# Kernel optimization log

Hardware: AMD Instinct MI355X
Metric: run time of the kernel (lower is better)

## Reference

```python
import jax, jax.numpy as jnp
import numpy as np

NUM_USERS = 1024
NUM_BUSINESSES = 2048
N_NODES = NUM_USERS + NUM_BUSINESSES  # 3072
B = 1024            # batch size (== NUM_USERS to keep the business_idx-offset bug valid)
E = 16384           # edges (self loops added inside reference, PyG GATConv default)
H = 768             # hidden_size
HEADS = 8
NUM_IMAGES = 3


def setup_inputs() -> dict:
    key = jax.random.key(0)
    ks = jax.random.split(key, 24)
    def rn(k, shape, s=0.02):
        return jax.random.normal(k, shape, dtype=jnp.float32) * s
    inp = {
        'text_cls': rn(ks[0], (B, 768), 1.0),              # BERT CLS features
        'img_cls': rn(ks[1], (B, NUM_IMAGES, 768), 1.0),   # ViT CLS features per image
        'biz_feats': rn(ks[2], (B, 3), 1.0),
        'W_text': rn(ks[3], (768, H)), 'b_text': jnp.zeros((H,), jnp.float32),
        'W_img': rn(ks[4], (768, H)), 'b_img': jnp.zeros((H,), jnp.float32),
        'W_bf': rn(ks[5], (3, H)), 'b_bf': jnp.zeros((H,), jnp.float32),
        'user_table': rn(ks[6], (NUM_USERS, H)),
        'biz_table': rn(ks[7], (NUM_BUSINESSES, H)),
        'W1': rn(ks[8], (H, HEADS * H)),
        'att_src1': rn(ks[9], (HEADS, H), 0.1),
        'att_dst1': rn(ks[10], (HEADS, H), 0.1),
        'b1': jnp.zeros((HEADS * H,), jnp.float32),
        'W2': rn(ks[11], (HEADS * H, H)),
        'att_src2': rn(ks[12], (1, H), 0.1),
        'att_dst2': rn(ks[13], (1, H), 0.1),
        'b2': jnp.zeros((H,), jnp.float32),
        'Wf1': rn(ks[14], (4 * H, 2 * H)), 'bf1': jnp.zeros((2 * H,), jnp.float32),
        'Wf2': rn(ks[15], (2 * H, H)), 'bf2': jnp.zeros((H,), jnp.float32),
        'Wf3': rn(ks[16], (H, 1)), 'bf3': jnp.zeros((1,), jnp.float32),
        'user_idx': jax.random.randint(ks[17], (B,), 0, NUM_USERS),
        'business_idx': jax.random.randint(ks[18], (B,), NUM_USERS, N_NODES),
        'edge_index': jax.random.randint(ks[19], (2, E), 0, N_NODES),
    }
    return inp


def gat_conv(x, src, dst, W, a_src, a_dst, bias, heads):
    # PyG GATConv: linear -> per-head additive attention -> scatter softmax over dst -> scatter add
    N = x.shape[0]
    C = W.shape[1] // heads
    h = (x @ W).reshape(N, heads, C)                       # [N,H,C]
    s_src = jnp.sum(h * a_src, axis=-1)                    # [N,H]
    s_dst = jnp.sum(h * a_dst, axis=-1)                    # [N,H]
    e = jax.nn.leaky_relu(s_src[src] + s_dst[dst], 0.2)    # [E,H]
    e_max = jax.ops.segment_max(e, dst, num_segments=N)    # [N,H]
    ee = jnp.exp(e - e_max[dst])
    denom = jax.ops.segment_sum(ee, dst, num_segments=N)   # [N,H]
    alpha = ee / (denom[dst] + 1e-16)                      # [E,H]
    out = jax.ops.segment_sum(h[src] * alpha[..., None], dst, num_segments=N)  # [N,H,C]
    return out.reshape(N, heads * C) + bias


def reference(text_cls, img_cls, biz_feats, W_text, b_text, W_img, b_img, W_bf, b_bf,
              user_table, biz_table, W1, att_src1, att_dst1, b1, W2, att_src2, att_dst2, b2,
              Wf1, bf1, Wf2, bf2, Wf3, bf3, user_idx, business_idx, edge_index):
    text_emb = text_cls @ W_text + b_text                       # TextEncoder.fc
    img_emb = jnp.mean(img_cls, axis=1) @ W_img + b_img         # ImageEncoder mean + fc
    meta = biz_feats @ W_bf + b_bf                              # business_feature_fc
    user_emb = user_table[user_idx]
    biz_emb = biz_table[business_idx - user_idx.shape[0]]       # faithful: offset by batch size
    x = jnp.zeros((N_NODES, H), jnp.float32)
    x = x.at[user_idx].set(user_emb)
    x = x.at[business_idx].set((text_emb + img_emb + meta + biz_emb) / 4.0)
    loop = jnp.arange(N_NODES)
    src = jnp.concatenate([edge_index[0], loop])                # add self loops (PyG default)
    dst = jnp.concatenate([edge_index[1], loop])
    x = jax.nn.relu(gat_conv(x, src, dst, W1, att_src1, att_dst1, b1, HEADS))
    x = gat_conv(x, src, dst, W2, att_src2, att_dst2, b2, 1)
    cat = jnp.concatenate([x[user_idx], x[business_idx], text_emb, img_emb], axis=1)  # [B,4H]
    h1 = jax.nn.relu(cat @ Wf1 + bf1)
    h2 = jax.nn.relu(h1 @ Wf2 + bf2)
    return (h2 @ Wf3 + bf3).squeeze(-1)                         # [B]
```

## Files before the change

kernel.cpp:

```cpp
#include <hip/hip_runtime.h>
#include <hip/hip_bf16.h>

namespace {

constexpr int kB = 1024;
constexpr int kNU = 1024;
constexpr int kNB = 2048;
constexpr int kNN = 3072;
constexpr int kE = 16384;
constexpr int kET = kE + kNN;
constexpr int kH = 768;
constexpr int kHeads = 8;
constexpr int kS2 = 8;

typedef __attribute__((ext_vector_type(8))) short bf16x8_t;
typedef __attribute__((ext_vector_type(4))) float f32x4_t;

__device__ __forceinline__ float tof(float x) { return x; }
__device__ __forceinline__ float tof(__hip_bfloat16 x) { return __bfloat162float(x); }
__device__ __forceinline__ void stor(float* p, float v) { *p = v; }
__device__ __forceinline__ void stor(__hip_bfloat16* p, float v) { *p = __float2bfloat16(v); }

__device__ __forceinline__ float blo(unsigned u) {
  union { unsigned u; float f; } c; c.u = u << 16; return c.f;
}
__device__ __forceinline__ float bhi(unsigned u) {
  union { unsigned u; float f; } c; c.u = u & 0xffff0000u; return c.f;
}

__device__ __forceinline__ unsigned pk2(float a, float b) {
  union { __hip_bfloat16 h[2]; unsigned u; } c;
  c.h[0] = __float2bfloat16(a); c.h[1] = __float2bfloat16(b);
  return c.u;
}

__device__ __forceinline__ void gload_lds16(const void* g, void* l) {
  __builtin_amdgcn_global_load_lds(
      (const __attribute__((address_space(1))) void*)g,
      (__attribute__((address_space(3))) void*)l, 16, 0, 0);
}

template <int BM, int BN, int FM, int FN, typename TC>
__device__ __forceinline__ void gemm_body(
    const __hip_bfloat16* __restrict__ A, const __hip_bfloat16* __restrict__ Bt,
    const float* __restrict__ bias, TC* __restrict__ C,
    int K, int lda, int ldc, int act, int bx, int by) {
  __shared__ __align__(16) __hip_bfloat16 As[2][BM][32];
  __shared__ __align__(16) __hip_bfloat16 Bs[2][BN][32];
  const int t = threadIdx.x;
  const int w = t >> 6, lane = t & 63;
  const int wm = w >> 1, wn = w & 1;
  const int bm = by * BM, bn = bx * BN;
  const int lr = lane & 15, lg = lane >> 4;

  f32x4_t acc[FM][FN];
#pragma unroll
  for (int m = 0; m < FM; ++m)
#pragma unroll
    for (int n = 0; n < FN; ++n) acc[m][n] = (f32x4_t){0.f, 0.f, 0.f, 0.f};

  auto stage = [&](int buf, int kt) {
    const int k0 = kt << 5;
#pragma unroll
    for (int i = 0; i < BM / 64; ++i) {
      int L = i * 256 + t;
      gload_lds16(A + (size_t)(bm + (L >> 2)) * lda + k0 + (L & 3) * 8,
                  (char*)(&As[buf][0][0]) + ((size_t)(i * 256 + w * 64)) * 16);
    }
#pragma unroll
    for (int i = 0; i < BN / 64; ++i) {
      int L = i * 256 + t;
      gload_lds16(Bt + (size_t)(bn + (L >> 2)) * K + k0 + (L & 3) * 8,
                  (char*)(&Bs[buf][0][0]) + ((size_t)(i * 256 + w * 64)) * 16);
    }
  };

  const int NT = K >> 5;
  stage(0, 0);
  __syncthreads();
  for (int kt = 0; kt < NT; ++kt) {
    const int cur = kt & 1;
    if (kt + 1 < NT) stage(cur ^ 1, kt + 1);
    bf16x8_t af[FM], bv[FN];
#pragma unroll
    for (int m = 0; m < FM; ++m)
      af[m] = *(const bf16x8_t*)&As[cur][wm * FM * 16 + m * 16 + lr][lg * 8];
#pragma unroll
    for (int n = 0; n < FN; ++n)
      bv[n] = *(const bf16x8_t*)&Bs[cur][wn * FN * 16 + n * 16 + lr][lg * 8];
#pragma unroll
    for (int m = 0; m < FM; ++m)
#pragma unroll
      for (int n = 0; n < FN; ++n)
        acc[m][n] = __builtin_amdgcn_mfma_f32_16x16x32_bf16(af[m], bv[n], acc[m][n], 0, 0, 0);
    __syncthreads();
  }

#pragma unroll
  for (int m = 0; m < FM; ++m) {
    const int row0 = bm + wm * FM * 16 + m * 16 + lg * 4;
#pragma unroll
    for (int n = 0; n < FN; ++n) {
      const int cn = bn + wn * FN * 16 + n * 16 + lr;
      const float bvv = bias ? bias[cn] : 0.f;
#pragma unroll
      for (int r = 0; r < 4; ++r) {
        float v = acc[m][n][r] + bvv;
        if (act) v = fmaxf(v, 0.f);
        stor(&C[(size_t)(row0 + r) * ldc + cn], v);
      }
    }
  }
}

__device__ __forceinline__ void swz_xy(bool mfast, int& bx, int& by) {
  const int nwg = gridDim.x * gridDim.y;
  const int orig = blockIdx.y * gridDim.x + blockIdx.x;
  const int swz = (orig & 7) * (nwg >> 3) + (orig >> 3);
  if (mfast) { by = swz % gridDim.y; bx = swz / gridDim.y; }
  else       { bx = swz % gridDim.x; by = swz / gridDim.x; }
}

template <int BM, int BN, int FM, int FN>
__global__ __launch_bounds__(256) void mfma_gemm_dual(
    const __hip_bfloat16* __restrict__ A0, const __hip_bfloat16* __restrict__ Bt0,
    const float* __restrict__ bias0, float* __restrict__ C0,
    const __hip_bfloat16* __restrict__ A1, const __hip_bfloat16* __restrict__ Bt1,
    const float* __restrict__ bias1, float* __restrict__ C1,
    int N, int K) {
  int bx, by;
  swz_xy(true, bx, by);
  const __hip_bfloat16* A = blockIdx.z ? A1 : A0;
  const __hip_bfloat16* Bt = blockIdx.z ? Bt1 : Bt0;
  const float* bias = blockIdx.z ? bias1 : bias0;
  float* C = blockIdx.z ? C1 : C0;
  gemm_body<BM, BN, FM, FN, float>(A, Bt, bias, C, K, K, N, 0, bx, by);
}

template <int BM, int BN, int FM, int FN>
__global__ __launch_bounds__(256) void gemm_head(
    const __hip_bfloat16* __restrict__ y, const __hip_bfloat16* __restrict__ W1t,
    const float* __restrict__ b1, __hip_bfloat16* __restrict__ x2) {
  const int hd = blockIdx.x;
  const int tile = blockIdx.y;
  const int bx = tile % (kH / BN);
  const int by = tile / (kH / BN);
  gemm_body<BM, BN, FM, FN, __hip_bfloat16>(
      y + (size_t)hd * kH, W1t + (size_t)hd * kH * kH, b1 + hd * kH,
      x2 + (size_t)hd * kH, kH, kHeads * kH, kHeads * kH, 1, bx, by);
}

template <int BM, int BN, int FM, int FN, int S>
__global__ __launch_bounds__(256) void mfma_gemm_kpin(
    const __hip_bfloat16* __restrict__ A, const __hip_bfloat16* __restrict__ Bt,
    __hip_bfloat16* __restrict__ Cpart, int M, int N, int K) {
  __shared__ __align__(16) __hip_bfloat16 As[2][BM][32];
  __shared__ __align__(16) __hip_bfloat16 Bs[2][BN][32];
  const int kc = blockIdx.x;
  const int tile = blockIdx.y;
  const int tilesN = N / BN;
  const int bx = tile % tilesN;
  const int by = tile / tilesN;
  const int KC = K / S;
  const int kbeg = kc * KC;
  const int t = threadIdx.x;
  const int w = t >> 6, lane = t & 63;
  const int wm = w >> 1, wn = w & 1;
  const int bm = by * BM, bn = bx * BN;
  const int lr = lane & 15, lg = lane >> 4;

  f32x4_t acc[FM][FN];
#pragma unroll
  for (int m = 0; m < FM; ++m)
#pragma unroll
    for (int n = 0; n < FN; ++n) acc[m][n] = (f32x4_t){0.f, 0.f, 0.f, 0.f};

  auto stage = [&](int buf, int kt) {
    const int k0 = kbeg + (kt << 5);
#pragma unroll
    for (int i = 0; i < BM / 64; ++i) {
      int L = i * 256 + t;
      gload_lds16(A + (size_t)(bm + (L >> 2)) * K + k0 + (L & 3) * 8,
                  (char*)(&As[buf][0][0]) + ((size_t)(i * 256 + w * 64)) * 16);
    }
#pragma unroll
    for (int i = 0; i < BN / 64; ++i) {
      int L = i * 256 + t;
      gload_lds16(Bt + (size_t)(bn + (L >> 2)) * K + k0 + (L & 3) * 8,
                  (char*)(&Bs[buf][0][0]) + ((size_t)(i * 256 + w * 64)) * 16);
    }
  };

  const int NT = KC >> 5;
  stage(0, 0);
  __syncthreads();
  for (int kt = 0; kt < NT; ++kt) {
    const int cur = kt & 1;
    if (kt + 1 < NT) stage(cur ^ 1, kt + 1);
    bf16x8_t af[FM], bv[FN];
#pragma unroll
    for (int m = 0; m < FM; ++m)
      af[m] = *(const bf16x8_t*)&As[cur][wm * FM * 16 + m * 16 + lr][lg * 8];
#pragma unroll
    for (int n = 0; n < FN; ++n)
      bv[n] = *(const bf16x8_t*)&Bs[cur][wn * FN * 16 + n * 16 + lr][lg * 8];
#pragma unroll
    for (int m = 0; m < FM; ++m)
#pragma unroll
      for (int n = 0; n < FN; ++n)
        acc[m][n] = __builtin_amdgcn_mfma_f32_16x16x32_bf16(af[m], bv[n], acc[m][n], 0, 0, 0);
    __syncthreads();
  }

  __hip_bfloat16* Cp = Cpart + (size_t)kc * M * N;
#pragma unroll
  for (int m = 0; m < FM; ++m) {
    const int row0 = bm + wm * FM * 16 + m * 16 + lg * 4;
#pragma unroll
    for (int n = 0; n < FN; ++n) {
      const int cn = bn + wn * FN * 16 + n * 16 + lr;
#pragma unroll
      for (int r = 0; r < 4; ++r)
        Cp[(size_t)(row0 + r) * N + cn] = __float2bfloat16(acc[m][n][r]);
    }
  }
}

template <int BM, int BN, int FM, int FN>
__global__ __launch_bounds__(256) void mfma_gemm_splitk(
    const __hip_bfloat16* __restrict__ A, const __hip_bfloat16* __restrict__ Bt,
    float* __restrict__ Cpart, int M, int N, int K, int KC) {
  __shared__ __align__(16) __hip_bfloat16 As[2][BM][32];
  __shared__ __align__(16) __hip_bfloat16 Bs[2][BN][32];
  int bx, by;
  swz_xy(false, bx, by);
  const int t = threadIdx.x;
  const int w = t >> 6, lane = t & 63;
  const int wm = w >> 1, wn = w & 1;
  const int bm = by * BM, bn = bx * BN;
  const int kbeg = blockIdx.z * KC;
  const int lr = lane & 15, lg = lane >> 4;

  f32x4_t acc[FM][FN];
#pragma unroll
  for (int m = 0; m < FM; ++m)
#pragma unroll
    for (int n = 0; n < FN; ++n) acc[m][n] = (f32x4_t){0.f, 0.f, 0.f, 0.f};

  auto stage = [&](int buf, int kt) {
    const int k0 = kbeg + (kt << 5);
#pragma unroll
    for (int i = 0; i < BM / 64; ++i) {
      int L = i * 256 + t;
      gload_lds16(A + (size_t)(bm + (L >> 2)) * K + k0 + (L & 3) * 8,
                  (char*)(&As[buf][0][0]) + ((size_t)(i * 256 + w * 64)) * 16);
    }
#pragma unroll
    for (int i = 0; i < BN / 64; ++i) {
      int L = i * 256 + t;
      gload_lds16(Bt + (size_t)(bn + (L >> 2)) * K + k0 + (L & 3) * 8,
                  (char*)(&Bs[buf][0][0]) + ((size_t)(i * 256 + w * 64)) * 16);
    }
  };

  const int NT = KC >> 5;
  stage(0, 0);
  __syncthreads();
  for (int kt = 0; kt < NT; ++kt) {
    const int cur = kt & 1;
    if (kt + 1 < NT) stage(cur ^ 1, kt + 1);
    bf16x8_t af[FM], bv[FN];
#pragma unroll
    for (int m = 0; m < FM; ++m)
      af[m] = *(const bf16x8_t*)&As[cur][wm * FM * 16 + m * 16 + lr][lg * 8];
#pragma unroll
    for (int n = 0; n < FN; ++n)
      bv[n] = *(const bf16x8_t*)&Bs[cur][wn * FN * 16 + n * 16 + lr][lg * 8];
#pragma unroll
    for (int m = 0; m < FM; ++m)
#pragma unroll
      for (int n = 0; n < FN; ++n)
        acc[m][n] = __builtin_amdgcn_mfma_f32_16x16x32_bf16(af[m], bv[n], acc[m][n], 0, 0, 0);
    __syncthreads();
  }

  float* Cp = Cpart + (size_t)blockIdx.z * M * N;
#pragma unroll
  for (int m = 0; m < FM; ++m) {
    const int row0 = bm + wm * FM * 16 + m * 16 + lg * 4;
#pragma unroll
    for (int n = 0; n < FN; ++n) {
      const int cn = bn + wn * FN * 16 + n * 16 + lr;
#pragma unroll
      for (int r = 0; r < 4; ++r) Cp[(size_t)(row0 + r) * N + cn] = acc[m][n][r];
    }
  }
}

__global__ __launch_bounds__(192) void reduce_scores2_kernel(
    const __hip_bfloat16* __restrict__ part, const float* __restrict__ att_src,
    const float* __restrict__ att_dst, __hip_bfloat16* __restrict__ h2,
    float* __restrict__ s_src, float* __restrict__ s_dst) {
  __shared__ float redS[3], redD[3];
  const int row = blockIdx.x;
  const int t = threadIdx.x;
  const int c = t * 4;
  const __hip_bfloat16* p = part + (size_t)row * kH + c;
  float a0 = 0.f, a1 = 0.f, a2 = 0.f, a3 = 0.f;
#pragma unroll
  for (int z = 0; z < kS2; ++z) {
    uint2 v = *(const uint2*)(p + (size_t)z * kNN * kH);
    a0 += blo(v.x); a1 += bhi(v.x); a2 += blo(v.y); a3 += bhi(v.y);
  }
  __hip_bfloat16 b0 = __float2bfloat16(a0), b1 = __float2bfloat16(a1);
  __hip_bfloat16 b2 = __float2bfloat16(a2), b3 = __float2bfloat16(a3);
  __hip_bfloat16* o = h2 + (size_t)row * kH + c;
  o[0] = b0; o[1] = b1; o[2] = b2; o[3] = b3;
  float f0 = tof(b0), f1 = tof(b1), f2 = tof(b2), f3 = tof(b3);
  float ss = f0 * att_src[c] + f1 * att_src[c + 1] + f2 * att_src[c + 2] + f3 * att_src[c + 3];
  float sd = f0 * att_dst[c] + f1 * att_dst[c + 1] + f2 * att_dst[c + 2] + f3 * att_dst[c + 3];
#pragma unroll
  for (int off = 32; off; off >>= 1) { ss += __shfl_down(ss, off); sd += __shfl_down(sd, off); }
  if ((t & 63) == 0) { redS[t >> 6] = ss; redD[t >> 6] = sd; }
  __syncthreads();
  if (t == 0) {
    s_src[row] = redS[0] + redS[1] + redS[2];
    s_dst[row] = redD[0] + redD[1] + redD[2];
  }
}

__global__ void reduce_relu_kernel(const float* __restrict__ part,
                                   const float* __restrict__ bias,
                                   __hip_bfloat16* __restrict__ outb, int MN4, int N) {
  int i = blockIdx.x * 256 + threadIdx.x;
  if (i >= MN4) return;
  float4 s = ((const float4*)part)[i];
  float4 p = ((const float4*)part)[(size_t)MN4 + i];
  int c = (i * 4) % N;
  float v0 = fmaxf(s.x + p.x + bias[c], 0.f);
  float v1 = fmaxf(s.y + p.y + bias[c + 1], 0.f);
  float v2 = fmaxf(s.z + p.z + bias[c + 2], 0.f);
  float v3 = fmaxf(s.w + p.w + bias[c + 3], 0.f);
  uint2 o;
  o.x = pk2(v0, v1); o.y = pk2(v2, v3);
  *(uint2*)(outb + (size_t)i * 4) = o;
}

__global__ __launch_bounds__(192) void reduce_final_kernel(
    const float* __restrict__ part, const float* __restrict__ bias,
    const float* __restrict__ Wf3, const float* __restrict__ bf3,
    float* __restrict__ out) {
  __shared__ float red[3];
  const int row = blockIdx.x;
  const int t = threadIdx.x;
  const int c = t * 4;
  const float* p0 = part + (size_t)row * kH + c;
  const float* p1 = p0 + (size_t)kB * kH;
  float4 a = *(const float4*)p0;
  float4 b = *(const float4*)p1;
  float v0 = fmaxf(a.x + b.x + bias[c], 0.f);
  float v1 = fmaxf(a.y + b.y + bias[c + 1], 0.f);
  float v2 = fmaxf(a.z + b.z + bias[c + 2], 0.f);
  float v3 = fmaxf(a.w + b.w + bias[c + 3], 0.f);
  float s = v0 * Wf3[c] + v1 * Wf3[c + 1] + v2 * Wf3[c + 2] + v3 * Wf3[c + 3];
#pragma unroll
  for (int off = 32; off; off >>= 1) s += __shfl_down(s, off);
  if ((t & 63) == 0) red[t >> 6] = s;
  __syncthreads();
  if (t == 0) out[row] = red[0] + red[1] + red[2] + bf3[0];
}

struct TJobs {
  const float* in[6];
  __hip_bfloat16* out[6];
  int K[6];
  int N[6];
  int start[7];
};

__global__ __launch_bounds__(256) void transp_prep_kernel(
    TJobs j, const float* __restrict__ text_cls, const float* __restrict__ img_cls,
    __hip_bfloat16* __restrict__ text_bf, __hip_bfloat16* __restrict__ imgm_bf,
    int prep_blocks, const float* __restrict__ W1, const float* __restrict__ a_src,
    const float* __restrict__ a_dst, float* __restrict__ wa,
    int wa_blocks, uint4* __restrict__ xb4) {
  __shared__ float tl[32][33];
  const int bid = blockIdx.x;
  const int t = threadIdx.x;
  if (bid >= j.start[6] + prep_blocks + wa_blocks) {
    int i = (bid - j.start[6] - prep_blocks - wa_blocks) * 256 + t;
    if (i < kNN * kH * 2 / 16) xb4[i] = (uint4){0u, 0u, 0u, 0u};
    return;
  }
  if (bid >= j.start[6] + prep_blocks) {
    int gw = ((bid - j.start[6] - prep_blocks) * 256 + t) >> 6;
    int lane = t & 63;
    if (gw >= kHeads * kH) return;
    int i = gw >> 3, hd = gw & 7;
    const float* wrow = W1 + (size_t)i * (kHeads * kH) + hd * kH;
    const float* as = a_src + (size_t)hd * kH;
    const float* ad = a_dst + (size_t)hd * kH;
    float ss = 0.f, sd = 0.f;
    for (int c = lane; c < kH; c += 64) {
      float wv = wrow[c];
      ss = fmaf(wv, as[c], ss);
      sd = fmaf(wv, ad[c], sd);
    }
#pragma unroll
    for (int o = 32; o; o >>= 1) { ss += __shfl_down(ss, o); sd += __shfl_down(sd, o); }
    if (lane == 0) {
      wa[hd * kH + i] = ss;
      wa[kHeads * kH + hd * kH + i] = sd;
    }
    return;
  }
  if (bid >= j.start[6]) {
    int idx = (bid - j.start[6]) * 256 + t;
    if (idx < kB * kH) {
      text_bf[idx] = __float2bfloat16(text_cls[idx]);
      int b = idx / kH, c = idx - b * kH;
      const float* p = img_cls + (size_t)b * 3 * kH + c;
      imgm_bf[idx] = __float2bfloat16((p[0] + p[kH] + p[2 * kH]) * (1.f / 3.f));
    }
    return;
  }
  int idx = 0;
#pragma unroll
  for (int q = 1; q < 6; ++q)
    if (bid >= j.start[q]) idx = q;
  const int tile = bid - j.start[idx];
  const int N = j.N[idx], K = j.K[idx];
  const int tilesN = N >> 5;
  const int n0 = (tile % tilesN) << 5, k0 = (tile / tilesN) << 5;
  const float* in = j.in[idx];
  __hip_bfloat16* out = j.out[idx];
  const int r = t >> 3, c = (t & 7) * 4;
#pragma unroll
  for (int i = 0; i < 4; ++i) tl[r][c + i] = in[(size_t)(k0 + r) * N + n0 + c + i];
  __syncthreads();
  __hip_bfloat16* op = out + (size_t)(n0 + r) * K + k0 + c;
#pragma unroll
  for (int i = 0; i < 4; ++i) op[i] = __float2bfloat16(tl[c + i][r]);
}

__global__ __launch_bounds__(256) void s1_kernel(const __hip_bfloat16* __restrict__ xb,
                                                 const float* __restrict__ wa,
                                                 float* __restrict__ s1s,
                                                 float* __restrict__ s1d) {
  __shared__ unsigned xrow[kH / 2];
  const int n = blockIdx.x;
  const int t = threadIdx.x;
  const unsigned* xp = (const unsigned*)(xb + (size_t)n * kH);
  if (t < 128) { xrow[t] = xp[t]; xrow[t + 128] = xp[t + 128]; xrow[t + 256] = xp[t + 256]; }
  __syncthreads();
  const int w = t >> 6, lane = t & 63;
  const float* ws0 = wa + (size_t)w * kH;
  const float* wd0 = wa + (size_t)(kHeads + w) * kH;
  const float* ws1 = wa + (size_t)(w + 4) * kH;
  const float* wd1 = wa + (size_t)(kHeads + w + 4) * kH;
  float s0 = 0.f, d0 = 0.f, s1 = 0.f, d1 = 0.f;
  for (int u = lane; u < kH / 2; u += 64) {
    unsigned v = xrow[u];
    float f0 = blo(v), f1 = bhi(v);
    int c = u * 2;
    s0 = fmaf(f0, ws0[c], fmaf(f1, ws0[c + 1], s0));
    d0 = fmaf(f0, wd0[c], fmaf(f1, wd0[c + 1], d0));
    s1 = fmaf(f0, ws1[c], fmaf(f1, ws1[c + 1], s1));
    d1 = fmaf(f0, wd1[c], fmaf(f1, wd1[c + 1], d1));
  }
#pragma unroll
  for (int o = 32; o; o >>= 1) {
    s0 += __shfl_down(s0, o); d0 += __shfl_down(d0, o);
    s1 += __shfl_down(s1, o); d1 += __shfl_down(d1, o);
  }
  if (lane == 0) {
    s1s[n * 8 + w] = s0;     s1d[n * 8 + w] = d0;
    s1s[n * 8 + w + 4] = s1; s1d[n * 8 + w + 4] = d1;
  }
}

__global__ __launch_bounds__(256) void agg1x_kernel(
    const int* __restrict__ rowptr, const int* __restrict__ cols,
    const float* __restrict__ s1s, const float* __restrict__ s1d,
    const __hip_bfloat16* __restrict__ xb, __hip_bfloat16* __restrict__ y) {
  __shared__ float mh[8], rdh[8], sdl[8];
  __shared__ float alph[128][9];
  const int n = blockIdx.x;
  const int t = threadIdx.x, w = t >> 6, lane = t & 63;
  const int beg = rowptr[n], end = rowptr[n + 1];
  if (t < 8) sdl[t] = s1d[n * 8 + t];
  __syncthreads();
#pragma unroll
  for (int p = 0; p < 2; ++p) {
    const int h = w + p * 4;
    const float sd = sdl[h];
    float m = -3.402823466e38f;
    for (int i = beg + lane; i < end; i += 64) {
      float e = s1s[(size_t)cols[i] * 8 + h] + sd;
      e = (e > 0.f) ? e : 0.2f * e;
      m = fmaxf(m, e);
    }
#pragma unroll
    for (int o = 32; o; o >>= 1) m = fmaxf(m, __shfl_xor(m, o));
    float ds = 0.f;
    for (int i = beg + lane; i < end; i += 64) {
      float e = s1s[(size_t)cols[i] * 8 + h] + sd;
      e = (e > 0.f) ? e : 0.2f * e;
      ds += expf(e - m);
    }
#pragma unroll
    for (int o = 32; o; o >>= 1) ds += __shfl_xor(ds, o);
    if (lane == 0) { mh[h] = m; rdh[h] = 1.f / (ds + 1e-16f); }
  }
  __syncthreads();

  float acc[8][4];
#pragma unroll
  for (int h = 0; h < 8; ++h)
#pragma unroll
    for (int q = 0; q < 4; ++q) acc[h][q] = 0.f;
  const int c0 = t * 4;

  for (int chunk = beg; chunk < end; chunk += 128) {
    const int cnt = min(128, end - chunk);
#pragma unroll
    for (int p = 0; p < 2; ++p) {
      const int h = w + p * 4;
      const float sd = sdl[h], m = mh[h], rd = rdh[h];
      for (int i = lane; i < cnt; i += 64) {
        float e = s1s[(size_t)cols[chunk + i] * 8 + h] + sd;
        e = (e > 0.f) ? e : 0.2f * e;
        alph[i][h] = expf(e - m) * rd;
      }
    }
    __syncthreads();
    if (t < 192) {
      for (int i = 0; i < cnt; ++i) {
        int src = cols[chunk + i];
        uint2 v = *(const uint2*)(xb + (size_t)src * kH + c0);
        float f0 = blo(v.x), f1 = bhi(v.x), f2 = blo(v.y), f3 = bhi(v.y);
#pragma unroll
        for (int h = 0; h < 8; ++h) {
          float a = alph[i][h];
          acc[h][0] = fmaf(a, f0, acc[h][0]);
          acc[h][1] = fmaf(a, f1, acc[h][1]);
          acc[h][2] = fmaf(a, f2, acc[h][2]);
          acc[h][3] = fmaf(a, f3, acc[h][3]);
        }
      }
    }
    __syncthreads();
  }
  if (t < 192) {
#pragma unroll
    for (int h = 0; h < 8; ++h) {
      uint2 o;
      o.x = pk2(acc[h][0], acc[h][1]);
      o.y = pk2(acc[h][2], acc[h][3]);
      *(uint2*)(y + ((size_t)n * 8 + h) * kH + c0) = o;
    }
  }
}

__global__ __launch_bounds__(1024) void scan_kernel(const int* __restrict__ ei,
                                                    int* __restrict__ rowptr,
                                                    int* __restrict__ cursor) {
  __shared__ int sdeg[kNN];
  __shared__ int sums[1024];
  int t = threadIdx.x;
#pragma unroll
  for (int i = 0; i < 3; ++i) sdeg[t * 3 + i] = 0;
  __syncthreads();
  for (int e = t; e < kET; e += 1024) {
    int dst = (e < kE) ? ei[kE + e] : (e - kE);
    atomicAdd(&sdeg[dst], 1);
  }
  __syncthreads();
  int v0 = sdeg[t * 3], v1 = sdeg[t * 3 + 1], v2 = sdeg[t * 3 + 2];
  int s = v0 + v1 + v2;
  sums[t] = s;
  __syncthreads();
  for (int o = 1; o < 1024; o <<= 1) {
    int xv = (t >= o) ? sums[t - o] : 0;
    __syncthreads();
    sums[t] += xv;
    __syncthreads();
  }
  int excl = sums[t] - s;
  rowptr[t * 3] = excl;          cursor[t * 3] = excl;
  rowptr[t * 3 + 1] = excl + v0; cursor[t * 3 + 1] = excl + v0;
  rowptr[t * 3 + 2] = excl + v0 + v1; cursor[t * 3 + 2] = excl + v0 + v1;
  if (t == 1023) rowptr[kNN] = excl + s;
}

constexpr int kFillBlocks = (kET + 255) / 256;

__global__ __launch_bounds__(256) void fill_build_kernel(
    const int* __restrict__ ei, int* __restrict__ cursor, int* __restrict__ cols,
    const int* __restrict__ user_idx, const float* __restrict__ user_table,
    const int* __restrict__ business_idx, const float* __restrict__ text_emb,
    const float* __restrict__ img_emb, const float* __restrict__ biz_feats,
    const float* __restrict__ W_bf, const float* __restrict__ b_bf,
    const float* __restrict__ biz_table, __hip_bfloat16* __restrict__ xb) {
  const int bid = blockIdx.x;
  if (bid < kFillBlocks) {
    int e = bid * 256 + threadIdx.x;
    if (e >= kET) return;
    int src, dst;
    if (e < kE) { src = ei[e]; dst = ei[kE + e]; } else { src = dst = e - kE; }
    int pos = atomicAdd(&cursor[dst], 1);
    cols[pos] = src;
    return;
  }
  const int b = bid - kFillBlocks;
  if (b < kNU) {
    int node = user_idx[b];
    for (int c = threadIdx.x; c < kH; c += 256)
      xb[(size_t)node * kH + c] = __float2bfloat16(user_table[(size_t)node * kH + c]);
  } else {
    const int m = b - kNU;
    int cand = -1;
    for (int i = threadIdx.x; i < kB; i += 256)
      if (business_idx[i] == kNU + m) cand = i;
#pragma unroll
    for (int o = 32; o; o >>= 1) cand = max(cand, __shfl_xor(cand, o));
    __shared__ int red[4];
    if ((threadIdx.x & 63) == 0) red[threadIdx.x >> 6] = cand;
    __syncthreads();
    const int w = max(max(red[0], red[1]), max(red[2], red[3]));
    if (w < 0) return;
    int node = kNU + m;
    float f0 = biz_feats[w * 3], f1 = biz_feats[w * 3 + 1], f2 = biz_feats[w * 3 + 2];
    for (int c = threadIdx.x; c < kH; c += 256) {
      float meta = f0 * W_bf[c] + f1 * W_bf[kH + c] + f2 * W_bf[2 * kH + c] + b_bf[c];
      float v = (text_emb[(size_t)w * kH + c] + img_emb[(size_t)w * kH + c] + meta +
                 biz_table[(size_t)m * kH + c]) * 0.25f;
      xb[(size_t)node * kH + c] = __float2bfloat16(v);
    }
  }
}

__global__ __launch_bounds__(256) void gat_agg_kernel(
    const int* __restrict__ rowptr, const int* __restrict__ cols,
    const float* __restrict__ s_src, const float* __restrict__ s_dst,
    const __hip_bfloat16* __restrict__ h, const float* __restrict__ bias,
    float* __restrict__ out_f, int total) {
  const int pair = blockIdx.x * 4 + (threadIdx.x >> 6);
  if (pair >= total) return;
  const int lane = threadIdx.x & 63;
  const int n = pair;
  const int beg = rowptr[n], end = rowptr[n + 1];
  const float sdv = s_dst[pair];

  float m = -3.402823466e38f;
  for (int i = beg + lane; i < end; i += 64) {
    float e = s_src[cols[i]] + sdv;
    e = (e > 0.f) ? e : 0.2f * e;
    m = fmaxf(m, e);
  }
#pragma unroll
  for (int o = 32; o; o >>= 1) m = fmaxf(m, __shfl_xor(m, o));

  float dsum = 0.f;
  for (int i = beg + lane; i < end; i += 64) {
    float e = s_src[cols[i]] + sdv;
    e = (e > 0.f) ? e : 0.2f * e;
    dsum += expf(e - m);
  }
#pragma unroll
  for (int o = 32; o; o >>= 1) dsum += __shfl_xor(dsum, o);
  const float rdsum = 1.f / (dsum + 1e-16f);

  float a[12];
#pragma unroll
  for (int q = 0; q < 12; ++q) a[q] = 0.f;
  const size_t hoff = (size_t)lane * 4;
  for (int i = beg; i < end; ++i) {
    int src = cols[i];
    float e = s_src[src] + sdv;
    e = (e > 0.f) ? e : 0.2f * e;
    float wgt = expf(e - m) * rdsum;
    const __hip_bfloat16* hp = h + (size_t)src * kH + hoff;
#pragma unroll
    for (int j = 0; j < 3; ++j) {
      uint2 v = *(const uint2*)(hp + j * 256);
      a[j * 4 + 0] = fmaf(wgt, blo(v.x), a[j * 4 + 0]);
      a[j * 4 + 1] = fmaf(wgt, bhi(v.x), a[j * 4 + 1]);
      a[j * 4 + 2] = fmaf(wgt, blo(v.y), a[j * 4 + 2]);
      a[j * 4 + 3] = fmaf(wgt, bhi(v.y), a[j * 4 + 3]);
    }
  }
  const size_t ob = (size_t)n * kH + hoff;
#pragma unroll
  for (int j = 0; j < 3; ++j) {
#pragma unroll
    for (int q = 0; q < 4; ++q)
      out_f[ob + j * 256 + q] = a[j * 4 + q] + bias[hoff + j * 256 + q];
  }
}

__global__ void cat_kernel(const float* __restrict__ xf, const float* __restrict__ text_emb,
                           const float* __restrict__ img_emb, const int* __restrict__ user_idx,
                           const int* __restrict__ business_idx, __hip_bfloat16* __restrict__ cat) {
  int b = blockIdx.x;
  int u = user_idx[b], z = business_idx[b];
  __hip_bfloat16* crow = cat + (size_t)b * 4 * kH;
  for (int c = threadIdx.x; c < kH; c += blockDim.x) {
    crow[c] = __float2bfloat16(xf[(size_t)u * kH + c]);
    crow[kH + c] = __float2bfloat16(xf[(size_t)z * kH + c]);
    crow[2 * kH + c] = __float2bfloat16(text_emb[(size_t)b * kH + c]);
    crow[3 * kH + c] = __float2bfloat16(img_emb[(size_t)b * kH + c]);
  }
}

}

extern "C" void kernel_launch(void* const* d_in, const int* in_sizes, int n_in,
                              void* d_out, int out_size, void* d_ws, size_t ws_size,
                              hipStream_t stream) {
  const float* text_cls = (const float*)d_in[0];
  const float* img_cls = (const float*)d_in[1];
  const float* biz_feats = (const float*)d_in[2];
  const float* W_text = (const float*)d_in[3];
  const float* b_text = (const float*)d_in[4];
  const float* W_img = (const float*)d_in[5];
  const float* b_img = (const float*)d_in[6];
  const float* W_bf = (const float*)d_in[7];
  const float* b_bf = (const float*)d_in[8];
  const float* user_table = (const float*)d_in[9];
  const float* biz_table = (const float*)d_in[10];
  const float* W1 = (const float*)d_in[11];
  const float* att_src1 = (const float*)d_in[12];
  const float* att_dst1 = (const float*)d_in[13];
  const float* b1 = (const float*)d_in[14];
  const float* W2 = (const float*)d_in[15];
  const float* att_src2 = (const float*)d_in[16];
  const float* att_dst2 = (const float*)d_in[17];
  const float* b2 = (const float*)d_in[18];
  const float* Wf1 = (const float*)d_in[19];
  const float* bf1 = (const float*)d_in[20];
  const float* Wf2 = (const float*)d_in[21];
  const float* bf2 = (const float*)d_in[22];
  const float* Wf3 = (const float*)d_in[23];
  const float* bf3 = (const float*)d_in[24];
  const int* user_idx = (const int*)d_in[25];
  const int* business_idx = (const int*)d_in[26];
  const int* edge_index = (const int*)d_in[27];
  float* out = (float*)d_out;
  (void)in_sizes; (void)n_in; (void)out_size; (void)ws_size;

  char* base = (char*)d_ws;
  size_t off = 0;
  auto alloc = [&](size_t bytes) -> void* {
    void* p = base + off;
    off = (off + bytes + 255) & ~(size_t)255;
    return p;
  };
  __hip_bfloat16* xb = (__hip_bfloat16*)alloc((size_t)kNN * kH * 2);
  __hip_bfloat16* text_bf = (__hip_bfloat16*)alloc((size_t)kB * kH * 2);
  __hip_bfloat16* imgm_bf = (__hip_bfloat16*)alloc((size_t)kB * kH * 2);
  float* text_emb = (float*)alloc((size_t)kB * kH * 4);
  float* img_emb = (float*)alloc((size_t)kB * kH * 4);
  __hip_bfloat16* Wtt = (__hip_bfloat16*)alloc((size_t)kH * kH * 2);
  __hip_bfloat16* Wit = (__hip_bfloat16*)alloc((size_t)kH * kH * 2);
  __hip_bfloat16* W1t = (__hip_bfloat16*)alloc((size_t)kHeads * kH * kH * 2);
  __hip_bfloat16* W2t = (__hip_bfloat16*)alloc((size_t)kH * kHeads * kH * 2);
  __hip_bfloat16* Wf1t = (__hip_bfloat16*)alloc((size_t)2 * kH * 4 * kH * 2);
  __hip_bfloat16* Wf2t = (__hip_bfloat16*)alloc((size_t)kH * 2 * kH * 2);
  float* wa = (float*)alloc((size_t)2 * kHeads * kH * 4);
  __hip_bfloat16* y = (__hip_bfloat16*)alloc((size_t)kNN * kHeads * kH * 2);
  char* ext = (char*)alloc(9437184 + 6291456 + 3145728);
  __hip_bfloat16* part = (__hip_bfloat16*)y;
  float* xf = (float*)ext;
  __hip_bfloat16* catb = (__hip_bfloat16*)(ext + 9437184);
  __hip_bfloat16* m1 = (__hip_bfloat16*)(ext + 9437184 + 6291456);
  __hip_bfloat16* x2 = (__hip_bfloat16*)alloc((size_t)kNN * kHeads * kH * 2);
  __hip_bfloat16* h2 = (__hip_bfloat16*)alloc((size_t)kNN * kH * 2);
  float* s1s = (float*)alloc((size_t)kNN * kHeads * 4);
  float* s1d = (float*)alloc((size_t)kNN * kHeads * 4);
  float* s2s = (float*)alloc((size_t)kNN * 4);
  float* s2d = (float*)alloc((size_t)kNN * 4);
  int* rowptr = (int*)alloc((size_t)(kNN + 1) * 4);
  int* cursor = (int*)alloc((size_t)kNN * 4);
  int* cols = (int*)alloc((size_t)kET * 4);

  TJobs tj;
  tj.in[0] = W_text; tj.out[0] = Wtt;  tj.K[0] = kH;          tj.N[0] = kH;
  tj.in[1] = W_img;  tj.out[1] = Wit;  tj.K[1] = kH;          tj.N[1] = kH;
  tj.in[2] = W1;     tj.out[2] = W1t;  tj.K[2] = kH;          tj.N[2] = kHeads * kH;
  tj.in[3] = W2;     tj.out[3] = W2t;  tj.K[3] = kHeads * kH; tj.N[3] = kH;
  tj.in[4] = Wf1;    tj.out[4] = Wf1t; tj.K[4] = 4 * kH;      tj.N[4] = 2 * kH;
  tj.in[5] = Wf2;    tj.out[5] = Wf2t; tj.K[5] = 2 * kH;      tj.N[5] = kH;
  tj.start[0] = 0;
  for (int q = 0; q < 6; ++q)
    tj.start[q + 1] = tj.start[q] + (tj.K[q] / 32) * (tj.N[q] / 32);
  const int prep_blocks = (kB * kH + 255) / 256;
  const int wa_blocks = (kHeads * kH) / 4;
  const int init_blocks = (kNN * kH * 2 / 16 + 255) / 256;
  transp_prep_kernel<<<tj.start[6] + prep_blocks + wa_blocks + init_blocks, 256, 0, stream>>>(
      tj, text_cls, img_cls, text_bf, imgm_bf, prep_blocks, W1, att_src1, att_dst1, wa,
      wa_blocks, (uint4*)xb);

  mfma_gemm_dual<64, 128, 2, 4><<<dim3(kH / 128, kB / 64, 2), 256, 0, stream>>>(
      text_bf, Wtt, b_text, text_emb, imgm_bf, Wit, b_img, img_emb, kH, kH);

  scan_kernel<<<1, 1024, 0, stream>>>(edge_index, rowptr, cursor);
  fill_build_kernel<<<kFillBlocks + kNN, 256, 0, stream>>>(
      edge_index, cursor, cols, user_idx, user_table, business_idx, text_emb, img_emb,
      biz_feats, W_bf, b_bf, biz_table, xb);

  s1_kernel<<<kNN, 256, 0, stream>>>(xb, wa, s1s, s1d);
  agg1x_kernel<<<kNN, 256, 0, stream>>>(rowptr, cols, s1s, s1d, xb, y);
  gemm_head<128, 128, 4, 4><<<dim3(kHeads, (kNN / 128) * (kH / 128)), 256, 0, stream>>>(
      y, W1t, b1, x2);

  mfma_gemm_kpin<128, 128, 4, 4, kS2>
      <<<dim3(kS2, (kNN / 128) * (kH / 128)), 256, 0, stream>>>(
          x2, W2t, part, kNN, kH, kHeads * kH);
  reduce_scores2_kernel<<<kNN, 192, 0, stream>>>(part, att_src2, att_dst2, h2, s2s, s2d);
  gat_agg_kernel<<<kNN / 4, 256, 0, stream>>>(rowptr, cols, s2s, s2d, h2, b2, xf, kNN);

  cat_kernel<<<kB, 256, 0, stream>>>(xf, text_emb, img_emb, user_idx, business_idx, catb);
  mfma_gemm_splitk<64, 128, 2, 4><<<dim3(2 * kH / 128, kB / 64, 2), 256, 0, stream>>>(
      catb, Wf1t, (float*)y, kB, 2 * kH, 4 * kH, 2 * kH);
  reduce_relu_kernel<<<(kB * 2 * kH / 4 + 255) / 256, 256, 0, stream>>>(
      (float*)y, bf1, m1, kB * 2 * kH / 4, 2 * kH);
  mfma_gemm_splitk<64, 128, 2, 4><<<dim3(kH / 128, kB / 64, 2), 256, 0, stream>>>(
      m1, Wf2t, (float*)y, kB, kH, 2 * kH, kH);
  reduce_final_kernel<<<kB, 192, 0, stream>>>((float*)y, bf2, Wf3, bf3, out);
}
```

Before: 255.7 us.

## Fuse graph prep, encoder GEMMs, node build and layer-1 scores into three kernels

The CSR degree scan moves into block 0 of the weight-transpose/prep kernel, and that kernel now also zeroes the score buffers. The text/image encoder GEMM, the edge fill, and the user-row build now share one launch. Business rows are built in their own launch. Each row builder computes the layer-1 attention scores straight from its row in shared memory, so the separate s1 pass and several launches go away. The trade-offs: the scan now runs on a single 256-thread block, and the score zeroing assumes s1s and s1d sit next to each other in memory.

```diff
diff --git a/kernel.cpp b/kernel.cpp
--- a/kernel.cpp
+++ b/kernel.cpp
@@ -119,22 +119,6 @@
   const int swz = (orig & 7) * (nwg >> 3) + (orig >> 3);
   if (mfast) { by = swz % gridDim.y; bx = swz / gridDim.y; }
   else       { bx = swz % gridDim.x; by = swz / gridDim.x; }
-}
-
-template <int BM, int BN, int FM, int FN>
-__global__ __launch_bounds__(256) void mfma_gemm_dual(
-    const __hip_bfloat16* __restrict__ A0, const __hip_bfloat16* __restrict__ Bt0,
-    const float* __restrict__ bias0, float* __restrict__ C0,
-    const __hip_bfloat16* __restrict__ A1, const __hip_bfloat16* __restrict__ Bt1,
-    const float* __restrict__ bias1, float* __restrict__ C1,
-    int N, int K) {
-  int bx, by;
-  swz_xy(true, bx, by);
-  const __hip_bfloat16* A = blockIdx.z ? A1 : A0;
-  const __hip_bfloat16* Bt = blockIdx.z ? Bt1 : Bt0;
-  const float* bias = blockIdx.z ? bias1 : bias0;
-  float* C = blockIdx.z ? C1 : C0;
-  gemm_body<BM, BN, FM, FN, float>(A, Bt, bias, C, K, K, N, 0, bx, by);
 }
 
 template <int BM, int BN, int FM, int FN>
@@ -370,6 +354,34 @@
   if (t == 0) out[row] = red[0] + red[1] + red[2] + bf3[0];
 }
 
+__device__ __forceinline__ void node_scores(const float* xrow, int node,
+                                            const float* __restrict__ wa,
+                                            float* __restrict__ s1s,
+                                            float* __restrict__ s1d, int t) {
+  const int w = t >> 6, lane = t & 63;
+  const float* ws0 = wa + (size_t)w * kH;
+  const float* wd0 = wa + (size_t)(kHeads + w) * kH;
+  const float* ws1 = wa + (size_t)(w + 4) * kH;
+  const float* wd1 = wa + (size_t)(kHeads + w + 4) * kH;
+  float s0 = 0.f, d0 = 0.f, s1v = 0.f, d1 = 0.f;
+  for (int c = lane; c < kH; c += 64) {
+    float f = xrow[c];
+    s0 = fmaf(f, ws0[c], s0);
+    d0 = fmaf(f, wd0[c], d0);
+    s1v = fmaf(f, ws1[c], s1v);
+    d1 = fmaf(f, wd1[c], d1);
+  }
+#pragma unroll
+  for (int o = 32; o; o >>= 1) {
+    s0 += __shfl_down(s0, o); d0 += __shfl_down(d0, o);
+    s1v += __shfl_down(s1v, o); d1 += __shfl_down(d1, o);
+  }
+  if (lane == 0) {
+    s1s[node * 8 + w] = s0;      s1d[node * 8 + w] = d0;
+    s1s[node * 8 + w + 4] = s1v; s1d[node * 8 + w + 4] = d1;
+  }
+}
+
 struct TJobs {
   const float* in[6];
   __hip_bfloat16* out[6];
@@ -378,22 +390,57 @@
   int start[7];
 };
 
-__global__ __launch_bounds__(256) void transp_prep_kernel(
+__global__ __launch_bounds__(256) void mega1_kernel(
     TJobs j, const float* __restrict__ text_cls, const float* __restrict__ img_cls,
     __hip_bfloat16* __restrict__ text_bf, __hip_bfloat16* __restrict__ imgm_bf,
     int prep_blocks, const float* __restrict__ W1, const float* __restrict__ a_src,
     const float* __restrict__ a_dst, float* __restrict__ wa,
-    int wa_blocks, uint4* __restrict__ xb4) {
+    int wa_blocks, uint4* __restrict__ xb4, uint4* __restrict__ s1sd4,
+    const int* __restrict__ ei, int* __restrict__ rowptr, int* __restrict__ cursor) {
   __shared__ float tl[32][33];
+  __shared__ int sdeg[kNN];
+  __shared__ int ssum[256];
   const int bid = blockIdx.x;
   const int t = threadIdx.x;
-  if (bid >= j.start[6] + prep_blocks + wa_blocks) {
-    int i = (bid - j.start[6] - prep_blocks - wa_blocks) * 256 + t;
+  if (bid == 0) {
+    for (int i = t; i < kNN; i += 256) sdeg[i] = 0;
+    __syncthreads();
+    for (int e = t; e < kET; e += 256) {
+      int dst = (e < kE) ? ei[kE + e] : (e - kE);
+      atomicAdd(&sdeg[dst], 1);
+    }
+    __syncthreads();
+    int loc[12];
+    int s = 0;
+#pragma unroll
+    for (int q = 0; q < 12; ++q) { loc[q] = sdeg[t * 12 + q]; s += loc[q]; }
+    ssum[t] = s;
+    __syncthreads();
+    for (int o = 1; o < 256; o <<= 1) {
+      int xv = (t >= o) ? ssum[t - o] : 0;
+      __syncthreads();
+      ssum[t] += xv;
+      __syncthreads();
+    }
+    int excl = ssum[t] - s;
+#pragma unroll
+    for (int q = 0; q < 12; ++q) {
+      rowptr[t * 12 + q] = excl;
+      cursor[t * 12 + q] = excl;
+      excl += loc[q];
+    }
+    if (t == 255) rowptr[kNN] = excl;
+    return;
+  }
+  const int b2 = bid - 1;
+  if (b2 >= j.start[6] + prep_blocks + wa_blocks) {
+    int i = (b2 - j.start[6] - prep_blocks - wa_blocks) * 256 + t;
     if (i < kNN * kH * 2 / 16) xb4[i] = (uint4){0u, 0u, 0u, 0u};
+    if (i < 2 * kNN * kHeads * 4 / 16) s1sd4[i] = (uint4){0u, 0u, 0u, 0u};
     return;
   }
-  if (bid >= j.start[6] + prep_blocks) {
-    int gw = ((bid - j.start[6] - prep_blocks) * 256 + t) >> 6;
+  if (b2 >= j.start[6] + prep_blocks) {
+    int gw = ((b2 - j.start[6] - prep_blocks) * 256 + t) >> 6;
     int lane = t & 63;
     if (gw >= kHeads * kH) return;
     int i = gw >> 3, hd = gw & 7;
@@ -414,8 +461,8 @@
     }
     return;
   }
-  if (bid >= j.start[6]) {
-    int idx = (bid - j.start[6]) * 256 + t;
+  if (b2 >= j.start[6]) {
+    int idx = (b2 - j.start[6]) * 256 + t;
     if (idx < kB * kH) {
       text_bf[idx] = __float2bfloat16(text_cls[idx]);
       int b = idx / kH, c = idx - b * kH;
@@ -427,8 +474,8 @@
   int idx = 0;
 #pragma unroll
   for (int q = 1; q < 6; ++q)
-    if (bid >= j.start[q]) idx = q;
-  const int tile = bid - j.start[idx];
+    if (b2 >= j.start[q]) idx = q;
+  const int tile = b2 - j.start[idx];
   const int N = j.N[idx], K = j.K[idx];
   const int tilesN = N >> 5;
   const int n0 = (tile % tilesN) << 5, k0 = (tile / tilesN) << 5;
@@ -443,40 +490,82 @@
   for (int i = 0; i < 4; ++i) op[i] = __float2bfloat16(tl[c + i][r]);
 }
 
-__global__ __launch_bounds__(256) void s1_kernel(const __hip_bfloat16* __restrict__ xb,
-                                                 const float* __restrict__ wa,
-                                                 float* __restrict__ s1s,
-                                                 float* __restrict__ s1d) {
-  __shared__ unsigned xrow[kH / 2];
-  const int n = blockIdx.x;
+constexpr int kEncBlocks = (kH / 128) * (kB / 64);
+constexpr int kFillBlocks = (kET + 255) / 256;
+
+__global__ __launch_bounds__(256) void mega2_kernel(
+    const __hip_bfloat16* __restrict__ text_bf, const __hip_bfloat16* __restrict__ Wtt,
+    const float* __restrict__ b_text, float* __restrict__ text_emb,
+    const __hip_bfloat16* __restrict__ imgm_bf, const __hip_bfloat16* __restrict__ Wit,
+    const float* __restrict__ b_img, float* __restrict__ img_emb,
+    const int* __restrict__ ei, int* __restrict__ cursor, int* __restrict__ cols,
+    const int* __restrict__ user_idx, const float* __restrict__ user_table,
+    const float* __restrict__ wa, __hip_bfloat16* __restrict__ xb,
+    float* __restrict__ s1s, float* __restrict__ s1d) {
+  __shared__ float xrow[kH];
+  const int bid = blockIdx.x;
   const int t = threadIdx.x;
-  const unsigned* xp = (const unsigned*)(xb + (size_t)n * kH);
-  if (t < 128) { xrow[t] = xp[t]; xrow[t + 128] = xp[t + 128]; xrow[t + 256] = xp[t + 256]; }
-  __syncthreads();
-  const int w = t >> 6, lane = t & 63;
-  const float* ws0 = wa + (size_t)w * kH;
-  const float* wd0 = wa + (size_t)(kHeads + w) * kH;
-  const float* ws1 = wa + (size_t)(w + 4) * kH;
-  const float* wd1 = wa + (size_t)(kHeads + w + 4) * kH;
-  float s0 = 0.f, d0 = 0.f, s1 = 0.f, d1 = 0.f;
-  for (int u = lane; u < kH / 2; u += 64) {
-    unsigned v = xrow[u];
-    float f0 = blo(v), f1 = bhi(v);
-    int c = u * 2;
-    s0 = fmaf(f0, ws0[c], fmaf(f1, ws0[c + 1], s0));
-    d0 = fmaf(f0, wd0[c], fmaf(f1, wd0[c + 1], d0));
-    s1 = fmaf(f0, ws1[c], fmaf(f1, ws1[c + 1], s1));
-    d1 = fmaf(f0, wd1[c], fmaf(f1, wd1[c + 1], d1));
-  }
-#pragma unroll
-  for (int o = 32; o; o >>= 1) {
-    s0 += __shfl_down(s0, o); d0 += __shfl_down(d0, o);
-    s1 += __shfl_down(s1, o); d1 += __shfl_down(d1, o);
-  }
-  if (lane == 0) {
-    s1s[n * 8 + w] = s0;     s1d[n * 8 + w] = d0;
-    s1s[n * 8 + w + 4] = s1; s1d[n * 8 + w + 4] = d1;
-  }
+  if (bid < 2 * kEncBlocks) {
+    const int p = bid / kEncBlocks, tile = bid % kEncBlocks;
+    const int bx = tile % (kH / 128), by = tile / (kH / 128);
+    const __hip_bfloat16* A = p ? imgm_bf : text_bf;
+    const __hip_bfloat16* Bt = p ? Wit : Wtt;
+    const float* bias = p ? b_img : b_text;
+    float* C = p ? img_emb : text_emb;
+    gemm_body<64, 128, 2, 4, float>(A, Bt, bias, C, kH, kH, kH, 0, bx, by);
+    return;
+  }
+  if (bid < 2 * kEncBlocks + kFillBlocks) {
+    int e = (bid - 2 * kEncBlocks) * 256 + t;
+    if (e >= kET) return;
+    int src, dst;
+    if (e < kE) { src = ei[e]; dst = ei[kE + e]; } else { src = dst = e - kE; }
+    int pos = atomicAdd(&cursor[dst], 1);
+    cols[pos] = src;
+    return;
+  }
+  const int b = bid - 2 * kEncBlocks - kFillBlocks;
+  const int node = user_idx[b];
+  for (int c = t; c < kH; c += 256) {
+    __hip_bfloat16 bf = __float2bfloat16(user_table[(size_t)node * kH + c]);
+    xb[(size_t)node * kH + c] = bf;
+    xrow[c] = tof(bf);
+  }
+  __syncthreads();
+  node_scores(xrow, node, wa, s1s, s1d, t);
+}
+
+__global__ __launch_bounds__(256) void mega3_kernel(
+    const int* __restrict__ business_idx, const float* __restrict__ text_emb,
+    const float* __restrict__ img_emb, const float* __restrict__ biz_feats,
+    const float* __restrict__ W_bf, const float* __restrict__ b_bf,
+    const float* __restrict__ biz_table, const float* __restrict__ wa,
+    __hip_bfloat16* __restrict__ xb, float* __restrict__ s1s, float* __restrict__ s1d) {
+  __shared__ int red[4];
+  __shared__ float xrow[kH];
+  const int m = blockIdx.x;
+  const int t = threadIdx.x;
+  int cand = -1;
+  for (int i = t; i < kB; i += 256)
+    if (business_idx[i] == kNU + m) cand = i;
+#pragma unroll
+  for (int o = 32; o; o >>= 1) cand = max(cand, __shfl_xor(cand, o));
+  if ((t & 63) == 0) red[t >> 6] = cand;
+  __syncthreads();
+  const int w = max(max(red[0], red[1]), max(red[2], red[3]));
+  if (w < 0) return;
+  const int node = kNU + m;
+  float f0 = biz_feats[w * 3], f1 = biz_feats[w * 3 + 1], f2 = biz_feats[w * 3 + 2];
+  for (int c = t; c < kH; c += 256) {
+    float meta = f0 * W_bf[c] + f1 * W_bf[kH + c] + f2 * W_bf[2 * kH + c] + b_bf[c];
+    float v = (text_emb[(size_t)w * kH + c] + img_emb[(size_t)w * kH + c] + meta +
+               biz_table[(size_t)m * kH + c]) * 0.25f;
+    __hip_bfloat16 bf = __float2bfloat16(v);
+    xb[(size_t)node * kH + c] = bf;
+    xrow[c] = tof(bf);
+  }
+  __syncthreads();
+  node_scores(xrow, node, wa, s1s, s1d, t);
 }
 
 __global__ __launch_bounds__(256) void agg1x_kernel(
@@ -558,84 +647,6 @@
       o.x = pk2(acc[h][0], acc[h][1]);
       o.y = pk2(acc[h][2], acc[h][3]);
       *(uint2*)(y + ((size_t)n * 8 + h) * kH + c0) = o;
-    }
-  }
-}
-
-__global__ __launch_bounds__(1024) void scan_kernel(const int* __restrict__ ei,
-                                                    int* __restrict__ rowptr,
-                                                    int* __restrict__ cursor) {
-  __shared__ int sdeg[kNN];
-  __shared__ int sums[1024];
-  int t = threadIdx.x;
-#pragma unroll
-  for (int i = 0; i < 3; ++i) sdeg[t * 3 + i] = 0;
-  __syncthreads();
-  for (int e = t; e < kET; e += 1024) {
-    int dst = (e < kE) ? ei[kE + e] : (e - kE);
-    atomicAdd(&sdeg[dst], 1);
-  }
-  __syncthreads();
-  int v0 = sdeg[t * 3], v1 = sdeg[t * 3 + 1], v2 = sdeg[t * 3 + 2];
-  int s = v0 + v1 + v2;
-  sums[t] = s;
-  __syncthreads();
-  for (int o = 1; o < 1024; o <<= 1) {
-    int xv = (t >= o) ? sums[t - o] : 0;
-    __syncthreads();
-    sums[t] += xv;
-    __syncthreads();
-  }
-  int excl = sums[t] - s;
-  rowptr[t * 3] = excl;          cursor[t * 3] = excl;
-  rowptr[t * 3 + 1] = excl + v0; cursor[t * 3 + 1] = excl + v0;
-  rowptr[t * 3 + 2] = excl + v0 + v1; cursor[t * 3 + 2] = excl + v0 + v1;
-  if (t == 1023) rowptr[kNN] = excl + s;
-}
-
-constexpr int kFillBlocks = (kET + 255) / 256;
-
-__global__ __launch_bounds__(256) void fill_build_kernel(
-    const int* __restrict__ ei, int* __restrict__ cursor, int* __restrict__ cols,
-    const int* __restrict__ user_idx, const float* __restrict__ user_table,
-    const int* __restrict__ business_idx, const float* __restrict__ text_emb,
-    const float* __restrict__ img_emb, const float* __restrict__ biz_feats,
-    const float* __restrict__ W_bf, const float* __restrict__ b_bf,
-    const float* __restrict__ biz_table, __hip_bfloat16* __restrict__ xb) {
-  const int bid = blockIdx.x;
-  if (bid < kFillBlocks) {
-    int e = bid * 256 + threadIdx.x;
-    if (e >= kET) return;
-    int src, dst;
-    if (e < kE) { src = ei[e]; dst = ei[kE + e]; } else { src = dst = e - kE; }
-    int pos = atomicAdd(&cursor[dst], 1);
-    cols[pos] = src;
-    return;
-  }
-  const int b = bid - kFillBlocks;
-  if (b < kNU) {
-    int node = user_idx[b];
-    for (int c = threadIdx.x; c < kH; c += 256)
-      xb[(size_t)node * kH + c] = __float2bfloat16(user_table[(size_t)node * kH + c]);
-  } else {
-    const int m = b - kNU;
-    int cand = -1;
-    for (int i = threadIdx.x; i < kB; i += 256)
-      if (business_idx[i] == kNU + m) cand = i;
-#pragma unroll
-    for (int o = 32; o; o >>= 1) cand = max(cand, __shfl_xor(cand, o));
-    __shared__ int red[4];
-    if ((threadIdx.x & 63) == 0) red[threadIdx.x >> 6] = cand;
-    __syncthreads();
-    const int w = max(max(red[0], red[1]), max(red[2], red[3]));
-    if (w < 0) return;
-    int node = kNU + m;
-    float f0 = biz_feats[w * 3], f1 = biz_feats[w * 3 + 1], f2 = biz_feats[w * 3 + 2];
-    for (int c = threadIdx.x; c < kH; c += 256) {
-      float meta = f0 * W_bf[c] + f1 * W_bf[kH + c] + f2 * W_bf[2 * kH + c] + b_bf[c];
-      float v = (text_emb[(size_t)w * kH + c] + img_emb[(size_t)w * kH + c] + meta +
-                 biz_table[(size_t)m * kH + c]) * 0.25f;
-      xb[(size_t)node * kH + c] = __float2bfloat16(v);
     }
   }
 }
@@ -783,6 +794,7 @@
   int* rowptr = (int*)alloc((size_t)(kNN + 1) * 4);
   int* cursor = (int*)alloc((size_t)kNN * 4);
   int* cols = (int*)alloc((size_t)kET * 4);
+  (void)s1d;
 
   TJobs tj;
   tj.in[0] = W_text; tj.out[0] = Wtt;  tj.K[0] = kH;          tj.N[0] = kH;
@@ -797,19 +809,17 @@
   const int prep_blocks = (kB * kH + 255) / 256;
   const int wa_blocks = (kHeads * kH) / 4;
   const int init_blocks = (kNN * kH * 2 / 16 + 255) / 256;
-  transp_prep_kernel<<<tj.start[6] + prep_blocks + wa_blocks + init_blocks, 256, 0, stream>>>(
+  mega1_kernel<<<1 + tj.start[6] + prep_blocks + wa_blocks + init_blocks, 256, 0, stream>>>(
       tj, text_cls, img_cls, text_bf, imgm_bf, prep_blocks, W1, att_src1, att_dst1, wa,
-      wa_blocks, (uint4*)xb);
-
-  mfma_gemm_dual<64, 128, 2, 4><<<dim3(kH / 128, kB / 64, 2), 256, 0, stream>>>(
-      text_bf, Wtt, b_text, text_emb, imgm_bf, Wit, b_img, img_emb, kH, kH);
-
-  scan_kernel<<<1, 1024, 0, stream>>>(edge_index, rowptr, cursor);
-  fill_build_kernel<<<kFillBlocks + kNN, 256, 0, stream>>>(
-      edge_index, cursor, cols, user_idx, user_table, business_idx, text_emb, img_emb,
-      biz_feats, W_bf, b_bf, biz_table, xb);
-
-  s1_kernel<<<kNN, 256, 0, stream>>>(xb, wa, s1s, s1d);
+      wa_blocks, (uint4*)xb, (uint4*)s1s, edge_index, rowptr, cursor);
+
+  mega2_kernel<<<2 * kEncBlocks + kFillBlocks + kNU, 256, 0, stream>>>(
+      text_bf, Wtt, b_text, text_emb, imgm_bf, Wit, b_img, img_emb,
+      edge_index, cursor, cols, user_idx, user_table, wa, xb, s1s, s1d);
+
+  mega3_kernel<<<kNB, 256, 0, stream>>>(business_idx, text_emb, img_emb, biz_feats,
+                                        W_bf, b_bf, biz_table, wa, xb, s1s, s1d);
+
   agg1x_kernel<<<kNN, 256, 0, stream>>>(rowptr, cols, s1s, s1d, xb, y);
   gemm_head<128, 128, 4, 4><<<dim3(kHeads, (kNN / 128) * (kH / 128)), 256, 0, stream>>>(
       y, W1t, b1, x2);
```

Result: faster. 247.8 us (-3.1%).
